# Kernel optimization log

Measured on AMD Instinct MI355X. Metric: run time of the kernel, lower is better.

## Reference

```python
import jax, jax.numpy as jnp
import numpy as np

B, L, H, U = 4, 4096, 1024, 1024


def setup_inputs() -> dict:
    key = jax.random.key(0)
    k0, k1, k2, k3 = jax.random.split(key, 4)
    inputs = jax.random.normal(k0, (B, L, H), dtype=jnp.float32)
    # linear layer params (torch default init scale ~ 1/sqrt(fan_in))
    W_rkv = jax.random.normal(k1, (H, 3 * U), dtype=jnp.float32) / np.sqrt(H)
    b_rkv = jnp.zeros((3 * U,), dtype=jnp.float32)
    W_o = jax.random.normal(k2, (U, H), dtype=jnp.float32) / np.sqrt(U)
    b_o = jnp.zeros((H,), dtype=jnp.float32)
    # nu_log init exactly as in the torch module
    r_min, r_max = 0.9, 0.999
    u = jax.random.uniform(k3, (U,), dtype=jnp.float32)
    nu_log = jnp.log(-0.5 * jnp.log(u * (r_max ** 2 - r_min ** 2) + r_min ** 2))
    gamma_log = jnp.zeros((U,), dtype=jnp.float32)
    return {"inputs": inputs, "W_rkv": W_rkv, "b_rkv": b_rkv,
            "W_o": W_o, "b_o": b_o, "nu_log": nu_log, "gamma_log": gamma_log}


def reference(inputs, W_rkv, b_rkv, W_o, b_o, nu_log, gamma_log):
    # projections
    rkv = jnp.einsum('blh,hu->blu', inputs, W_rkv) + b_rkv  # [B,L,3U]
    r, k, v = jnp.split(rkv, 3, axis=-1)
    r = jax.nn.sigmoid(r)
    k = jnp.exp(k)
    kv = k * v
    u = jnp.concatenate([kv, k], axis=-1)                   # [B,L,2U]
    nu = jnp.exp(jnp.concatenate([nu_log, nu_log]))         # [2U]
    gamma = jnp.exp(nu_log + gamma_log) - 1.0               # [U]
    lam = jnp.exp(-nu)                                      # per-channel decay
    # The torch log-depth doubling scan computes the linear recurrence
    # y_t = lam * y_{t-1} + u_t (y_0 = u_0). Use an associative scan over L.
    a = jnp.broadcast_to(lam, u.shape)

    def combine(c1, c2):
        a1, x1 = c1
        a2, x2 = c2
        return (a1 * a2, x1 * a2 + x2)

    _, y = jax.lax.associative_scan(combine, (a, u), axis=1)  # [B,L,2U]
    u1, u2 = jnp.split(y, 2, axis=-1)
    x = (u1 + gamma * kv) / (u2 + gamma * k + 1e-6) * r       # [B,L,U]
    return jnp.einsum('blu,uh->blh', x, W_o) + b_o
```

## Files before the change

### kernel.cpp

```cpp
#include <hip/hip_runtime.h>
#include <hip/hip_bf16.h>
#include <cstdint>
#include <cstddef>

constexpr int NB = 4;
constexpr int NL = 4096;
constexpr int NH = 1024;
constexpr int NU = 1024;
constexpr int NM = NB * NL;
constexpr int NCHUNK = 32;
constexpr int CLEN = NL / NCHUNK;

typedef __bf16 bf16x8 __attribute__((ext_vector_type(8)));
typedef __bf16 bf16x4 __attribute__((ext_vector_type(4)));
typedef float  f32x4  __attribute__((ext_vector_type(4)));

__global__ __launch_bounds__(256) void cast_f32_to_bf16(
    const float* __restrict__ in, __bf16* __restrict__ out, int n4) {
  int stride = gridDim.x * 256;
  for (int i = blockIdx.x * 256 + threadIdx.x; i < n4; i += stride) {
    const float4 v = reinterpret_cast<const float4*>(in)[i];
    bf16x4 o;
    o[0] = (__bf16)v.x; o[1] = (__bf16)v.y; o[2] = (__bf16)v.z; o[3] = (__bf16)v.w;
    reinterpret_cast<bf16x4*>(out)[i] = o;
  }
}

__global__ __launch_bounds__(256) void transpose_cast(
    const float* __restrict__ W, __bf16* __restrict__ Wt, int K, int N) {
  __shared__ float tile[32][33];
  int tx = threadIdx.x, ty = threadIdx.y;
  int n0 = blockIdx.x * 32, k0 = blockIdx.y * 32;
  #pragma unroll
  for (int i = 0; i < 32; i += 8)
    tile[ty + i][tx] = W[(size_t)(k0 + ty + i) * N + n0 + tx];
  __syncthreads();
  #pragma unroll
  for (int i = 0; i < 32; i += 8)
    Wt[(size_t)(n0 + ty + i) * K + k0 + tx] = (__bf16)tile[tx][ty + i];
}


#define SBAR0 __builtin_amdgcn_sched_barrier(0)

template<int EPI>
__global__ __launch_bounds__(512, 2) void gemm256(
    const __bf16* __restrict__ A, const __bf16* __restrict__ Bt,
    int M, int N, int K,
    const float* __restrict__ bias,
    float* __restrict__ out_r, float* __restrict__ out_k, float* __restrict__ out_v,
    float* __restrict__ out_f32) {
  __shared__ __attribute__((aligned(16))) __bf16 sA[2][256 * 64];
  __shared__ __attribute__((aligned(16))) __bf16 sB[2][256 * 64];

  const int tid = threadIdx.x;
  const int lane = tid & 63;
  const int w = tid >> 6;
  const int wm = w >> 2, wn = w & 3;

  const int ntn = N >> 8;
  const int nwg = gridDim.x;
  const int bid = blockIdx.x;
  const int cpx = nwg >> 3;
  const int swz = (bid & 7) * cpx + (bid >> 3);
  const int mt = swz / ntn, nt = swz % ntn;
  const long m0 = (long)mt * 256;
  const long n0 = (long)nt * 256;
  const int KT = K >> 6;

  const int srow = lane >> 3;
  const int scol = ((lane & 7) ^ srow) << 4;

  auto stageA = [&](int bi, int qm, int t) {
    if (t >= KT) return;
    #pragma unroll
    for (int j = 0; j < 2; ++j) {
      int u = w * 2 + j;
      int row0 = (u < 8) ? (qm * 64 + u * 8) : (128 + qm * 64 + (u - 8) * 8);
      const char* src = (const char*)A + ((m0 + row0 + srow) * (long)K + (long)t * 64) * 2 + scol;
      __builtin_amdgcn_global_load_lds(
          (const __attribute__((address_space(1))) unsigned int*)src,
          (__attribute__((address_space(3))) unsigned int*)((char*)&sA[bi][0] + row0 * 128),
          16, 0, 0);
    }
  };
  auto stageB = [&](int bi, int qn, int t) {
    if (t >= KT) return;
    #pragma unroll
    for (int j = 0; j < 2; ++j) {
      int u = w * 2 + j;
      int row0 = (u >> 2) * 64 + qn * 32 + (u & 3) * 8;
      const char* src = (const char*)Bt + ((n0 + row0 + srow) * (long)K + (long)t * 64) * 2 + scol;
      __builtin_amdgcn_global_load_lds(
          (const __attribute__((address_space(1))) unsigned int*)src,
          (__attribute__((address_space(3))) unsigned int*)((char*)&sB[bi][0] + row0 * 128),
          16, 0, 0);
    }
  };

  f32x4 acc[8][4];
  #pragma unroll
  for (int i = 0; i < 8; ++i)
    #pragma unroll
    for (int j = 0; j < 4; ++j) acc[i][j] = (f32x4)0.f;

#define PHASE(QM, QN, STAGE_STMT)                                              \
  do {                                                                         \
    const char* sAb = (const char*)&sA[bi][0];                                 \
    const char* sBb = (const char*)&sB[bi][0];                                 \
    bf16x8 av[4][2], bv[2][2];                                                 \
    _Pragma("unroll")                                                          \
    for (int f = 0; f < 4; ++f) {                                              \
      _Pragma("unroll")                                                        \
      for (int ks = 0; ks < 2; ++ks) {                                         \
        int r = wm * 128 + ((QM) * 4 + f) * 16 + (lane & 15);                  \
        int c = ks * 64 + (lane & 48);                                         \
        av[f][ks] = *(const bf16x8*)(sAb + r * 128 + (c ^ ((r & 7) << 4)));    \
      }                                                                        \
    }                                                                          \
    _Pragma("unroll")                                                          \
    for (int g = 0; g < 2; ++g) {                                              \
      _Pragma("unroll")                                                        \
      for (int ks = 0; ks < 2; ++ks) {                                         \
        int r = wn * 64 + ((QN) * 2 + g) * 16 + (lane & 15);                   \
        int c = ks * 64 + (lane & 48);                                         \
        bv[g][ks] = *(const bf16x8*)(sBb + r * 128 + (c ^ ((r & 7) << 4)));    \
      }                                                                        \
    }                                                                          \
    STAGE_STMT;                                                                \
    SBAR0;                                                                     \
    __builtin_amdgcn_s_barrier();                                              \
    SBAR0;                                                                     \
    __builtin_amdgcn_s_setprio(1);                                             \
    _Pragma("unroll")                                                          \
    for (int f = 0; f < 4; ++f) {                                              \
      _Pragma("unroll")                                                        \
      for (int g = 0; g < 2; ++g) {                                            \
        acc[(QM) * 4 + f][(QN) * 2 + g] = __builtin_amdgcn_mfma_f32_16x16x32_bf16( \
            av[f][0], bv[g][0], acc[(QM) * 4 + f][(QN) * 2 + g], 0, 0, 0);     \
        acc[(QM) * 4 + f][(QN) * 2 + g] = __builtin_amdgcn_mfma_f32_16x16x32_bf16( \
            av[f][1], bv[g][1], acc[(QM) * 4 + f][(QN) * 2 + g], 0, 0, 0);     \
      }                                                                        \
    }                                                                          \
    __builtin_amdgcn_s_setprio(0);                                             \
    SBAR0;                                                                     \
  } while (0)

#define EBAR { __builtin_amdgcn_s_barrier(); SBAR0; }

  stageA(0, 0, 0); stageB(0, 0, 0); stageA(0, 1, 0); stageB(0, 1, 0);
  stageA(1, 0, 1); stageB(1, 0, 1);
  SBAR0;
  asm volatile("s_waitcnt vmcnt(4)" ::: "memory");
  EBAR;

  for (int t = 0; t < KT; ++t) {
    const int bi = t & 1;
    PHASE(0, 0, stageB(bi ^ 1, 1, t + 1)); EBAR;
    PHASE(1, 0, stageA(bi ^ 1, 1, t + 1)); EBAR;
    PHASE(0, 1, stageB(bi, 0, t + 2));     EBAR;
    PHASE(1, 1, stageA(bi, 0, t + 2));
    SBAR0;
    if (t < KT - 2) { asm volatile("s_waitcnt vmcnt(4)" ::: "memory"); }
    else            { asm volatile("s_waitcnt vmcnt(0)" ::: "memory"); }
    EBAR;
  }
#undef PHASE
#undef EBAR

  float bs[4];
  #pragma unroll
  for (int fn = 0; fn < 4; ++fn)
    bs[fn] = bias[n0 + wn * 64 + fn * 16 + (lane & 15)];

  #pragma unroll
  for (int fm = 0; fm < 8; ++fm) {
    #pragma unroll
    for (int fn = 0; fn < 4; ++fn) {
      #pragma unroll
      for (int rr = 0; rr < 4; ++rr) {
        long row = m0 + wm * 128 + fm * 16 + (lane >> 4) * 4 + rr;
        long col = n0 + wn * 64 + fn * 16 + (lane & 15);
        float val = acc[fm][fn][rr] + bs[fn];
        if constexpr (EPI == 0) {
          int reg = (int)(col >> 10);
          int u = (int)(col & 1023);
          size_t idx = (size_t)row * NU + u;
          if (reg == 0)      out_r[idx] = 1.f / (1.f + __expf(-val));
          else if (reg == 1) out_k[idx] = __expf(val);
          else               out_v[idx] = val;
        } else {
          out_f32[(size_t)row * N + col] = val;
        }
      }
    }
  }
}

__global__ __launch_bounds__(256) void scan_pass1(
    const float* __restrict__ kbuf, const float* __restrict__ vbuf,
    const float* __restrict__ nu_log,
    float* __restrict__ S1, float* __restrict__ S2) {
  int u = blockIdx.x * 256 + threadIdx.x;
  int c = blockIdx.y;
  int b = blockIdx.z;
  float lam = __expf(-__expf(nu_log[u]));
  size_t base = ((size_t)b * NL + (size_t)c * CLEN) * NU + u;
  float y1 = 0.f, y2 = 0.f;
  #pragma unroll 4
  for (int t = 0; t < CLEN; ++t) {
    float kk = kbuf[base + (size_t)t * NU];
    float vv = vbuf[base + (size_t)t * NU];
    y1 = fmaf(lam, y1, kk * vv);
    y2 = fmaf(lam, y2, kk);
  }
  size_t si = ((size_t)b * NCHUNK + c) * NU + u;
  S1[si] = y1;
  S2[si] = y2;
}

__global__ __launch_bounds__(256) void scan_combine(
    const float* __restrict__ S1, const float* __restrict__ S2,
    const float* __restrict__ nu_log,
    float* __restrict__ C1, float* __restrict__ C2) {
  int u = blockIdx.x * 256 + threadIdx.x;
  int b = blockIdx.y;
  float lamCL = __expf(-__expf(nu_log[u]) * (float)CLEN);
  float y1 = 0.f, y2 = 0.f;
  for (int c = 0; c < NCHUNK; ++c) {
    size_t si = ((size_t)b * NCHUNK + c) * NU + u;
    C1[si] = y1;
    C2[si] = y2;
    y1 = fmaf(lamCL, y1, S1[si]);
    y2 = fmaf(lamCL, y2, S2[si]);
  }
}

__global__ __launch_bounds__(256) void scan_pass2(
    const float* __restrict__ kbuf, const float* __restrict__ vbuf,
    const float* __restrict__ rbuf,
    const float* __restrict__ C1, const float* __restrict__ C2,
    const float* __restrict__ nu_log, const float* __restrict__ gamma_log,
    __bf16* __restrict__ xbuf) {
  int u = blockIdx.x * 256 + threadIdx.x;
  int c = blockIdx.y;
  int b = blockIdx.z;
  float lam = __expf(-__expf(nu_log[u]));
  float gamma = __expf(nu_log[u] + gamma_log[u]) - 1.f;
  size_t si = ((size_t)b * NCHUNK + c) * NU + u;
  float y1 = C1[si], y2 = C2[si];
  size_t base = ((size_t)b * NL + (size_t)c * CLEN) * NU + u;
  #pragma unroll 4
  for (int t = 0; t < CLEN; ++t) {
    size_t idx = base + (size_t)t * NU;
    float kk = kbuf[idx];
    float vv = vbuf[idx];
    float rr = rbuf[idx];
    float kv = kk * vv;
    y1 = fmaf(lam, y1, kv);
    y2 = fmaf(lam, y2, kk);
    float x = (y1 + gamma * kv) / (y2 + gamma * kk + 1e-6f) * rr;
    xbuf[idx] = (__bf16)x;
  }
}

extern "C" void kernel_launch(void* const* d_in, const int* in_sizes, int n_in,
                              void* d_out, int out_size, void* d_ws, size_t ws_size,
                              hipStream_t stream) {
  const float* inputs    = (const float*)d_in[0];
  const float* W_rkv     = (const float*)d_in[1];
  const float* b_rkv     = (const float*)d_in[2];
  const float* W_o       = (const float*)d_in[3];
  const float* b_o       = (const float*)d_in[4];
  const float* nu_log    = (const float*)d_in[5];
  const float* gamma_log = (const float*)d_in[6];
  float* out = (float*)d_out;

  char* ws = (char*)d_ws;
  size_t off = 0;
  __bf16* Abuf  = (__bf16*)(ws + off); off += (size_t)NM * NH * 2;
  __bf16* WrkvT = (__bf16*)(ws + off); off += (size_t)3 * NU * NH * 2;
  __bf16* WoT   = (__bf16*)(ws + off); off += (size_t)NH * NU * 2;
  float*  rbuf  = (float*)(ws + off);  off += (size_t)NM * NU * 4;
  float*  kbuf  = (float*)(ws + off);  off += (size_t)NM * NU * 4;
  float*  vbuf  = (float*)(ws + off);  off += (size_t)NM * NU * 4;
  float*  S1    = (float*)(ws + off);  off += (size_t)NB * NCHUNK * NU * 4;
  float*  S2    = (float*)(ws + off);  off += (size_t)NB * NCHUNK * NU * 4;
  float*  C1    = (float*)(ws + off);  off += (size_t)NB * NCHUNK * NU * 4;
  float*  C2    = (float*)(ws + off);  off += (size_t)NB * NCHUNK * NU * 4;
  __bf16* xbuf  = Abuf;

  cast_f32_to_bf16<<<2048, 256, 0, stream>>>(inputs, Abuf, (NM * NH) / 4);

  transpose_cast<<<dim3(3 * NU / 32, NH / 32), dim3(32, 8), 0, stream>>>(W_rkv, WrkvT, NH, 3 * NU);
  transpose_cast<<<dim3(NH / 32, NU / 32), dim3(32, 8), 0, stream>>>(W_o, WoT, NU, NH);

  gemm256<0><<<(NM / 256) * (3 * NU / 256), 512, 0, stream>>>(
      Abuf, WrkvT, NM, 3 * NU, NH, b_rkv, rbuf, kbuf, vbuf, nullptr);

  scan_pass1<<<dim3(NU / 256, NCHUNK, NB), 256, 0, stream>>>(kbuf, vbuf, nu_log, S1, S2);
  scan_combine<<<dim3(NU / 256, NB), 256, 0, stream>>>(S1, S2, nu_log, C1, C2);
  scan_pass2<<<dim3(NU / 256, NCHUNK, NB), 256, 0, stream>>>(
      kbuf, vbuf, rbuf, C1, C2, nu_log, gamma_log, xbuf);

  gemm256<1><<<(NM / 256) * (NH / 256), 512, 0, stream>>>(
      xbuf, WoT, NM, NH, NU, b_o, nullptr, nullptr, nullptr, out);
}
```

Baseline: 368.1 us.

## Store r/k/v intermediates in bf16 and double scan chunk count

The projection GEMM epilogue now writes r, k and v as bf16 instead of fp32, and both scan passes read bf16 and convert to float. This halves the memory traffic of the large intermediates written by the GEMM and re-read by the scan. The scan chunk count doubles to 64 for more parallelism in the scan passes, and the GEMM prologue waits for all loads before starting. Storing exp(k) in bf16 loses precision and may widen the error against the reference.

```diff
diff --git a/kernel.cpp b/kernel.cpp
--- a/kernel.cpp
+++ b/kernel.cpp
@@ -8,7 +8,7 @@
 constexpr int NH = 1024;
 constexpr int NU = 1024;
 constexpr int NM = NB * NL;
-constexpr int NCHUNK = 32;
+constexpr int NCHUNK = 64;
 constexpr int CLEN = NL / NCHUNK;
 
 typedef __bf16 bf16x8 __attribute__((ext_vector_type(8)));
@@ -48,7 +48,7 @@
     const __bf16* __restrict__ A, const __bf16* __restrict__ Bt,
     int M, int N, int K,
     const float* __restrict__ bias,
-    float* __restrict__ out_r, float* __restrict__ out_k, float* __restrict__ out_v,
+    __bf16* __restrict__ out_r, __bf16* __restrict__ out_k, __bf16* __restrict__ out_v,
     float* __restrict__ out_f32) {
   __shared__ __attribute__((aligned(16))) __bf16 sA[2][256 * 64];
   __shared__ __attribute__((aligned(16))) __bf16 sB[2][256 * 64];
@@ -106,8 +106,6 @@
 
 #define PHASE(QM, QN, STAGE_STMT)                                              \
   do {                                                                         \
-    const char* sAb = (const char*)&sA[bi][0];                                 \
-    const char* sBb = (const char*)&sB[bi][0];                                 \
     bf16x8 av[4][2], bv[2][2];                                                 \
     _Pragma("unroll")                                                          \
     for (int f = 0; f < 4; ++f) {                                              \
@@ -148,14 +146,19 @@
 
 #define EBAR { __builtin_amdgcn_s_barrier(); SBAR0; }
 
-  stageA(0, 0, 0); stageB(0, 0, 0); stageA(0, 1, 0); stageB(0, 1, 0);
-  stageA(1, 0, 1); stageB(1, 0, 1);
-  SBAR0;
-  asm volatile("s_waitcnt vmcnt(4)" ::: "memory");
+  stageA(0, 0, 0); SBAR0;
+  stageB(0, 0, 0); SBAR0;
+  stageA(0, 1, 0); SBAR0;
+  stageB(0, 1, 0); SBAR0;
+  stageA(1, 0, 1); SBAR0;
+  stageB(1, 0, 1); SBAR0;
+  asm volatile("s_waitcnt vmcnt(0)" ::: "memory");
   EBAR;
 
   for (int t = 0; t < KT; ++t) {
     const int bi = t & 1;
+    const char* sAb = (const char*)&sA[bi][0];
+    const char* sBb = (const char*)&sB[bi][0];
     PHASE(0, 0, stageB(bi ^ 1, 1, t + 1)); EBAR;
     PHASE(1, 0, stageA(bi ^ 1, 1, t + 1)); EBAR;
     PHASE(0, 1, stageB(bi, 0, t + 2));     EBAR;
@@ -186,9 +189,9 @@
           int reg = (int)(col >> 10);
           int u = (int)(col & 1023);
           size_t idx = (size_t)row * NU + u;
-          if (reg == 0)      out_r[idx] = 1.f / (1.f + __expf(-val));
-          else if (reg == 1) out_k[idx] = __expf(val);
-          else               out_v[idx] = val;
+          if (reg == 0)      out_r[idx] = (__bf16)(1.f / (1.f + __expf(-val)));
+          else if (reg == 1) out_k[idx] = (__bf16)__expf(val);
+          else               out_v[idx] = (__bf16)val;
         } else {
           out_f32[(size_t)row * N + col] = val;
         }
@@ -198,7 +201,7 @@
 }
 
 __global__ __launch_bounds__(256) void scan_pass1(
-    const float* __restrict__ kbuf, const float* __restrict__ vbuf,
+    const __bf16* __restrict__ kbuf, const __bf16* __restrict__ vbuf,
     const float* __restrict__ nu_log,
     float* __restrict__ S1, float* __restrict__ S2) {
   int u = blockIdx.x * 256 + threadIdx.x;
@@ -209,8 +212,8 @@
   float y1 = 0.f, y2 = 0.f;
   #pragma unroll 4
   for (int t = 0; t < CLEN; ++t) {
-    float kk = kbuf[base + (size_t)t * NU];
-    float vv = vbuf[base + (size_t)t * NU];
+    float kk = (float)kbuf[base + (size_t)t * NU];
+    float vv = (float)vbuf[base + (size_t)t * NU];
     y1 = fmaf(lam, y1, kk * vv);
     y2 = fmaf(lam, y2, kk);
   }
@@ -237,8 +240,8 @@
 }
 
 __global__ __launch_bounds__(256) void scan_pass2(
-    const float* __restrict__ kbuf, const float* __restrict__ vbuf,
-    const float* __restrict__ rbuf,
+    const __bf16* __restrict__ kbuf, const __bf16* __restrict__ vbuf,
+    const __bf16* __restrict__ rbuf,
     const float* __restrict__ C1, const float* __restrict__ C2,
     const float* __restrict__ nu_log, const float* __restrict__ gamma_log,
     __bf16* __restrict__ xbuf) {
@@ -253,9 +256,9 @@
   #pragma unroll 4
   for (int t = 0; t < CLEN; ++t) {
     size_t idx = base + (size_t)t * NU;
-    float kk = kbuf[idx];
-    float vv = vbuf[idx];
-    float rr = rbuf[idx];
+    float kk = (float)kbuf[idx];
+    float vv = (float)vbuf[idx];
+    float rr = (float)rbuf[idx];
     float kv = kk * vv;
     y1 = fmaf(lam, y1, kv);
     y2 = fmaf(lam, y2, kk);
@@ -281,9 +284,9 @@
   __bf16* Abuf  = (__bf16*)(ws + off); off += (size_t)NM * NH * 2;
   __bf16* WrkvT = (__bf16*)(ws + off); off += (size_t)3 * NU * NH * 2;
   __bf16* WoT   = (__bf16*)(ws + off); off += (size_t)NH * NU * 2;
-  float*  rbuf  = (float*)(ws + off);  off += (size_t)NM * NU * 4;
-  float*  kbuf  = (float*)(ws + off);  off += (size_t)NM * NU * 4;
-  float*  vbuf  = (float*)(ws + off);  off += (size_t)NM * NU * 4;
+  __bf16* rbuf  = (__bf16*)(ws + off); off += (size_t)NM * NU * 2;
+  __bf16* kbuf  = (__bf16*)(ws + off); off += (size_t)NM * NU * 2;
+  __bf16* vbuf  = (__bf16*)(ws + off); off += (size_t)NM * NU * 2;
   float*  S1    = (float*)(ws + off);  off += (size_t)NB * NCHUNK * NU * 4;
   float*  S2    = (float*)(ws + off);  off += (size_t)NB * NCHUNK * NU * 4;
   float*  C1    = (float*)(ws + off);  off += (size_t)NB * NCHUNK * NU * 4;
```

After: 367.1 us. No clear change (-0.3%).
